# Kernel tuning notes

Measured on AMD Instinct MI355X. Metric: run time of the kernel, lower is better.

## Reference

```python
import jax, jax.numpy as jnp
import numpy as np
from jax import lax

WINDOW_SIZE = 11
SIGMA = 1.5
MAX_VAL = 1.0
C1 = (MAX_VAL * 0.01) ** 2
C2 = (MAX_VAL * 0.03) ** 2


def _make_window(channel: int, k: int = WINDOW_SIZE, sigma: float = SIGMA) -> np.ndarray:
    x = np.arange(k, dtype=np.float64)
    g = np.exp(-((x - k // 2) ** 2) / (2.0 * sigma ** 2))
    g = (g / g.sum()).astype(np.float32)
    # rank-1 separable 3D window, built as dense [C,1,k,k,k] kernel (OIDHW, groups=C)
    w3 = g[:, None, None] * g[None, :, None] * g[None, None, :]
    return np.broadcast_to(w3, (channel, 1, k, k, k)).copy()


def _dwconv3d(x, kernel, pad):
    # depthwise 3D conv, SAME padding for odd kernel
    return lax.conv_general_dilated(
        x, kernel, window_strides=(1, 1, 1), padding=[(pad, pad)] * 3,
        dimension_numbers=("NCDHW", "OIDHW", "NCDHW"),
        feature_group_count=kernel.shape[0])


def setup_inputs() -> dict:
    key = jax.random.key(0)
    k1, k2 = jax.random.split(key)
    shape = (2, 4, 64, 160, 160)  # [B, C, D, H, W]
    img1 = jax.random.uniform(k1, shape, dtype=jnp.float32)
    img2 = jax.random.uniform(k2, shape, dtype=jnp.float32)
    return {"img1": img1, "img2": img2}


def reference(img1, img2):
    channel = img1.shape[1]
    window = jnp.asarray(_make_window(channel))
    pad = WINDOW_SIZE // 2
    # mask = ones_like(img1) in the original -> identity multiply, omitted
    mu1 = _dwconv3d(img1, window, pad)
    mu2 = _dwconv3d(img2, window, pad)
    mu1_sq = mu1 * mu1
    mu2_sq = mu2 * mu2
    mu1_mu2 = mu1 * mu2
    sigma1_sq = _dwconv3d(img1 * img1, window, pad) - mu1_sq
    sigma2_sq = _dwconv3d(img2 * img2, window, pad) - mu2_sq
    sigma12 = _dwconv3d(img1 * img2, window, pad) - mu1_mu2
    ssim_map = ((2.0 * mu1_mu2 + C1) * (2.0 * sigma12 + C2)) / (
        (mu1_sq + mu2_sq + C1) * (sigma1_sq + sigma2_sq + C2))
    ssim = jnp.mean(ssim_map, axis=(0, 2, 3, 4))  # per-channel SSIM, shape [C]
    return 1.0 - ssim
```

## Files before the change

### kernel.cpp

```cpp
#include <hip/hip_runtime.h>
#include <math.h>
#include <stdint.h>
#include <string.h>

typedef float v2f __attribute__((ext_vector_type(2)));

namespace {

constexpr int C_DIM = 4;
constexpr int D_DIM = 64;
constexpr int H_DIM = 160;
constexpr int W_DIM = 160;

constexpr int TH = 16;
constexpr int TW = 16;
constexpr int HALO = 5;
constexpr int EH = 26;
constexpr int EW = 26;
constexpr int QST = 27;
constexpr int MST = 17;
constexpr int NPIX = EH * EW;

constexpr int TILES_W = 10;
constexpr int TPC = 100;
constexpr int NBLOCKS = 2 * C_DIM * TPC;

constexpr float C1f = 1e-4f;
constexpr float C2f = 9e-4f;
constexpr float INV_N = 1.0f / (2.0f * 64.0f * 160.0f * 160.0f);

struct GW { double gd[11]; };

}

static __device__ __forceinline__ void pk_fma(v2f& acc, v2f x, double g) {
    asm("v_pk_fma_f32 %0, %1, %2, %0" : "+v"(acc) : "v"(x), "s"(g));
}

__global__ void finalize_kernel(const float* __restrict__ partial,
                                float* __restrict__ out) {
    const int tid = threadIdx.x;
    const int c = tid >> 6;
    const int lane = tid & 63;
    float s = 0.0f;
#pragma unroll
    for (int b = 0; b < 2; ++b) {
        const int base = (b * C_DIM + c) * TPC;
        s += partial[base + lane];
        if (lane < TPC - 64) s += partial[base + 64 + lane];
    }
#pragma unroll
    for (int off = 32; off > 0; off >>= 1) s += __shfl_down(s, off, 64);
    if (lane == 0 && c < C_DIM) out[c] = 1.0f - s * INV_N;
}

__global__ __launch_bounds__(256, 4) void ssim3d_kernel(
    const float* __restrict__ img1, const float* __restrict__ img2,
    float* __restrict__ partial, GW gwp) {

    const int bid = blockIdx.x;
    const int tile = bid % TPC;
    const int c = (bid / TPC) % C_DIM;
    const int b = bid / (TPC * C_DIM);
    const int h0 = (tile / TILES_W) * TH;
    const int w0 = (tile % TILES_W) * TW;

    const long planeHW = (long)H_DIM * W_DIM;
    const long volbase = (long)(b * C_DIM + c) * D_DIM * planeHW;
    const long org = volbase + (long)(h0 - HALO) * W_DIM + (w0 - HALO);
    const float* __restrict__ p1 = img1 + org;
    const float* __restrict__ p2 = img2 + org;

    const bool interior = (h0 >= HALO) && (h0 + TH + HALO <= H_DIM) &&
                          (w0 >= HALO) && (w0 + TW + HALO <= W_DIM);

    __shared__ float4 xyqp[2][EH][QST];
    __shared__ float4 mid[2][EH][MST];
    __shared__ float  rbuf[4];

    const int tid = threadIdx.x;

    int off_[3], loff_[3];
    unsigned okmask = 0;
#pragma unroll
    for (int k = 0; k < 3; ++k) {
        const int e = tid + k * 256;
        const int hh = e / EW;
        const int ww = e - hh * EW;
        off_[k] = hh * W_DIM + ww;
        loff_[k] = hh * QST + ww;
        const int gh = h0 - HALO + hh;
        const int gw = w0 - HALO + ww;
        if (((unsigned)gh < (unsigned)H_DIM) &&
            ((unsigned)gw < (unsigned)W_DIM))
            okmask |= 1u << k;
    }
    const bool live2 = (tid < NPIX - 512);

    auto fetch_slice = [&](int s, v2f lv[3]) {
        const long sb = (long)s * planeHW;
#pragma unroll
        for (int k = 0; k < 3; ++k) {
            lv[k] = (v2f){0.0f, 0.0f};
            const bool live = (k < 2) || live2;
            if (live && (interior || ((okmask >> k) & 1u))) {
                const long gi = sb + off_[k];
                lv[k].x = p1[gi];
                lv[k].y = p2[gi];
            }
        }
    };
    auto commit_slice = [&](int buf, const v2f lv[3]) {
        float4* base = &xyqp[buf][0][0];
#pragma unroll
        for (int k = 0; k < 3; ++k) {
            const bool live = (k < 2) || live2;
            if (live) {
                const float x = lv[k].x, y = lv[k].y;
                base[loff_[k]] = make_float4(x, y, fmaf(x, x, y * y), x * y);
            }
        }
    };

    const bool wactive = (tid < 208);
    const int whh = tid % 26;
    const int wg2 = (tid / 26) * 2;

    auto wconv = [&](int cur) {
        v2f a0 = {0.f,0.f}, a1 = {0.f,0.f};
        v2f q0 = {0.f,0.f}, q1 = {0.f,0.f};
#pragma unroll
        for (int t = 0; t < 12; ++t) {
            const float4 m = xyqp[cur][whh][wg2 + t];
            const v2f xv = {m.x, m.y};
            const v2f qp = {m.z, m.w};
            if (t <= 10) {
                pk_fma(a0, xv, gwp.gd[t]);
                pk_fma(q0, qp, gwp.gd[t]);
            }
            if (t >= 1) {
                pk_fma(a1, xv, gwp.gd[t-1]);
                pk_fma(q1, qp, gwp.gd[t-1]);
            }
        }
        mid[cur][whh][wg2]     = make_float4(a0.x, a0.y, q0.x, q0.y);
        mid[cur][whh][wg2 + 1] = make_float4(a1.x, a1.y, q1.x, q1.y);
    };

    const int hw = tid & 15;
    const int hy = tid >> 4;

    float accum = 0.0f;
    auto ssim_add = [&](v2f mxy, v2f mqp) {
        const float m1 = mxy.x, m2 = mxy.y;
        const float q = mqp.x, pp = mqp.y;
        const float m1s = m1 * m1;
        const float m2s = m2 * m2;
        const float m12 = m1 * m2;
        const float spp = q - m1s - m2s;
        const float s12 = pp - m12;
        const float num = (2.0f * m12 + C1f) * (2.0f * s12 + C2f);
        const float den = (m1s + m2s + C1f) * (spp + C2f);
        accum = fmaf(num, __builtin_amdgcn_rcpf(den), accum);
    };

    v2f w0xy[14], w0qp[14];
#pragma unroll
    for (int i = 0; i < 14; ++i) {
        w0xy[i] = (v2f){0.f, 0.f}; w0qp[i] = (v2f){0.f, 0.f};
    }

    {
        v2f lv[3];
        fetch_slice(0, lv);
        commit_slice(0, lv);
    }
    __syncthreads();

    for (int sb = 0; sb < D_DIM; sb += 4) {
#pragma unroll
        for (int u = 0; u < 4; ++u) {
            const int s = sb + u;
            v2f lv[3];
            const bool have_next = (s + 1 < D_DIM);
            if (have_next) fetch_slice(s + 1, lv);
            if (wactive) wconv(u & 1);
            if (have_next) commit_slice((u + 1) & 1, lv);
            __syncthreads();
            {
                v2f zx = {0.f,0.f}, zq = {0.f,0.f};
#pragma unroll
                for (int t = 0; t < 11; ++t) {
                    const float4 m = mid[u & 1][hy + t][hw];
                    const v2f ma = {m.x, m.y};
                    const v2f mb = {m.z, m.w};
                    pk_fma(zx, ma, gwp.gd[t]);
                    pk_fma(zq, mb, gwp.gd[t]);
                }
                w0xy[10 + u] = zx; w0qp[10 + u] = zq;
                if (s >= HALO) {
                    v2f mx0 = {0.f,0.f}, mq0 = {0.f,0.f};
#pragma unroll
                    for (int t = 0; t < 11; ++t) {
                        pk_fma(mx0, w0xy[u + t], gwp.gd[t]);
                        pk_fma(mq0, w0qp[u + t], gwp.gd[t]);
                    }
                    ssim_add(mx0, mq0);
                }
            }
        }
        {
#pragma unroll
            for (int k = 0; k < 10; ++k) {
                w0xy[k] = w0xy[k + 4]; w0qp[k] = w0qp[k + 4];
            }
        }
    }

    {
#pragma unroll
        for (int i = 10; i < 14; ++i) {
            w0xy[i] = (v2f){0.f, 0.f}; w0qp[i] = (v2f){0.f, 0.f};
        }
#pragma unroll
        for (int u2 = 0; u2 < 5; ++u2) {
            v2f mx0 = {0.f,0.f}, mq0 = {0.f,0.f};
#pragma unroll
            for (int t = 0; t < 11; ++t) {
                if (u2 + t <= 13) {
                    pk_fma(mx0, w0xy[u2 + t], gwp.gd[t]);
                    pk_fma(mq0, w0qp[u2 + t], gwp.gd[t]);
                }
            }
            ssim_add(mx0, mq0);
        }
    }

#pragma unroll
    for (int off = 32; off > 0; off >>= 1) accum += __shfl_down(accum, off, 64);
    const int wave = tid >> 6;
    const int lane = tid & 63;
    if (lane == 0) rbuf[wave] = accum;
    __syncthreads();
    if (tid == 0) partial[bid] = rbuf[0] + rbuf[1] + rbuf[2] + rbuf[3];
}

extern "C" void kernel_launch(void* const* d_in, const int* in_sizes, int n_in,
                              void* d_out, int out_size, void* d_ws, size_t ws_size,
                              hipStream_t stream) {
    const float* img1 = (const float*)d_in[0];
    const float* img2 = (const float*)d_in[1];
    float* out = (float*)d_out;
    float* partial = (float*)d_ws;

    GW gw;
    {
        double gd[11];
        double ssum = 0.0;
        for (int i = 0; i < 11; ++i) {
            const double t = (double)(i - 5);
            gd[i] = exp(-(t * t) / 4.5);
            ssum += gd[i];
        }
        for (int i = 0; i < 11; ++i) {
            const float gf = (float)(gd[i] / ssum);
            uint32_t ub;
            memcpy(&ub, &gf, 4);
            const uint64_t up = ((uint64_t)ub << 32) | ub;
            memcpy(&gw.gd[i], &up, 8);
        }
    }

    ssim3d_kernel<<<NBLOCKS, 256, 0, stream>>>(img1, img2, partial, gw);
    finalize_kernel<<<1, 256, 0, stream>>>(partial, out);
}
```

Before: 218.7 us.

## Split depth into two chunks per tile and single-buffer the input slice

Each (batch, channel, tile) block is split into two depth halves, so the grid has twice as many blocks. Each half recomputes a halo of slices (aligned down to a multiple of 4) so its sliding-window state is correct at the boundary, and the finalize kernel sums the extra partials. The double-buffered input slice array in shared memory becomes a single buffer, with an extra barrier per slice so the commit runs after the horizontal pass. Launch bounds are raised to 5 blocks per SM. The aim is better CU fill and occupancy, paid for with redundant halo slices and more synchronisation.

Measured after the change: 223.8 us. +2.4%, slower.

```diff
diff --git a/kernel.cpp b/kernel.cpp
--- a/kernel.cpp
+++ b/kernel.cpp
@@ -23,7 +23,9 @@
 
 constexpr int TILES_W = 10;
 constexpr int TPC = 100;
-constexpr int NBLOCKS = 2 * C_DIM * TPC;
+constexpr int D_SPLIT = 2;
+constexpr int DCH = D_DIM / D_SPLIT;
+constexpr int NBLOCKS = D_SPLIT * 2 * C_DIM * TPC;
 
 constexpr float C1f = 1e-4f;
 constexpr float C2f = 9e-4f;
@@ -44,8 +46,8 @@
     const int lane = tid & 63;
     float s = 0.0f;
 #pragma unroll
-    for (int b = 0; b < 2; ++b) {
-        const int base = (b * C_DIM + c) * TPC;
+    for (int r = 0; r < D_SPLIT * 2; ++r) {
+        const int base = (r * C_DIM + c) * TPC;
         s += partial[base + lane];
         if (lane < TPC - 64) s += partial[base + 64 + lane];
     }
@@ -54,16 +56,23 @@
     if (lane == 0 && c < C_DIM) out[c] = 1.0f - s * INV_N;
 }
 
-__global__ __launch_bounds__(256, 4) void ssim3d_kernel(
+__global__ __launch_bounds__(256, 5) void ssim3d_kernel(
     const float* __restrict__ img1, const float* __restrict__ img2,
     float* __restrict__ partial, GW gwp) {
 
     const int bid = blockIdx.x;
     const int tile = bid % TPC;
     const int c = (bid / TPC) % C_DIM;
-    const int b = bid / (TPC * C_DIM);
+    const int rest = bid / (TPC * C_DIM);
+    const int b = rest & 1;
+    const int dh = rest >> 1;
     const int h0 = (tile / TILES_W) * TH;
     const int w0 = (tile % TILES_W) * TW;
+
+    const int d_lo = dh * DCH;
+    const int s_base = (d_lo == 0) ? 0 : ((d_lo - HALO) & ~3);
+    const int s_hi = min(D_DIM - 1, d_lo + DCH - 1 + HALO);
+    const bool has_tail = (d_lo + DCH == D_DIM);
 
     const long planeHW = (long)H_DIM * W_DIM;
     const long volbase = (long)(b * C_DIM + c) * D_DIM * planeHW;
@@ -74,7 +83,7 @@
     const bool interior = (h0 >= HALO) && (h0 + TH + HALO <= H_DIM) &&
                           (w0 >= HALO) && (w0 + TW + HALO <= W_DIM);
 
-    __shared__ float4 xyqp[2][EH][QST];
+    __shared__ float4 xyqp[EH][QST];
     __shared__ float4 mid[2][EH][MST];
     __shared__ float  rbuf[4];
 
@@ -110,8 +119,8 @@
             }
         }
     };
-    auto commit_slice = [&](int buf, const v2f lv[3]) {
-        float4* base = &xyqp[buf][0][0];
+    auto commit_slice = [&](const v2f lv[3]) {
+        float4* base = &xyqp[0][0];
 #pragma unroll
         for (int k = 0; k < 3; ++k) {
             const bool live = (k < 2) || live2;
@@ -131,7 +140,7 @@
         v2f q0 = {0.f,0.f}, q1 = {0.f,0.f};
 #pragma unroll
         for (int t = 0; t < 12; ++t) {
-            const float4 m = xyqp[cur][whh][wg2 + t];
+            const float4 m = xyqp[whh][wg2 + t];
             const v2f xv = {m.x, m.y};
             const v2f qp = {m.z, m.w};
             if (t <= 10) {
@@ -170,23 +179,21 @@
         w0xy[i] = (v2f){0.f, 0.f}; w0qp[i] = (v2f){0.f, 0.f};
     }
 
-    {
-        v2f lv[3];
-        fetch_slice(0, lv);
-        commit_slice(0, lv);
-    }
+    v2f lv[3];
+    fetch_slice(s_base, lv);
+    commit_slice(lv);
     __syncthreads();
 
-    for (int sb = 0; sb < D_DIM; sb += 4) {
+    for (int sb = s_base; sb <= s_hi; sb += 4) {
 #pragma unroll
         for (int u = 0; u < 4; ++u) {
             const int s = sb + u;
-            v2f lv[3];
-            const bool have_next = (s + 1 < D_DIM);
+            if (s > s_hi) break;
+            const bool have_next = (s + 1 <= s_hi);
             if (have_next) fetch_slice(s + 1, lv);
             if (wactive) wconv(u & 1);
-            if (have_next) commit_slice((u + 1) & 1, lv);
             __syncthreads();
+            if (have_next) commit_slice(lv);
             {
                 v2f zx = {0.f,0.f}, zq = {0.f,0.f};
 #pragma unroll
@@ -198,7 +205,7 @@
                     pk_fma(zq, mb, gwp.gd[t]);
                 }
                 w0xy[10 + u] = zx; w0qp[10 + u] = zq;
-                if (s >= HALO) {
+                if (s >= d_lo + HALO) {
                     v2f mx0 = {0.f,0.f}, mq0 = {0.f,0.f};
 #pragma unroll
                     for (int t = 0; t < 11; ++t) {
@@ -208,6 +215,7 @@
                     ssim_add(mx0, mq0);
                 }
             }
+            __syncthreads();
         }
         {
 #pragma unroll
@@ -217,7 +225,7 @@
         }
     }
 
-    {
+    if (has_tail) {
 #pragma unroll
         for (int i = 10; i < 14; ++i) {
             w0xy[i] = (v2f){0.f, 0.f}; w0qp[i] = (v2f){0.f, 0.f};
```

## Store raw xy in single LDS buffer, compute squares in W-pass, 4 outputs per thread

Applied to the files above, without the earlier changes.

The input slice buffer shrinks from double-buffered float4 (x,y,q,p) to a single-buffered v2f of raw values. The squared and product terms are now recomputed inside the W-direction convolution. Each W-pass thread produces four outputs instead of two, so only 104 threads are active there, which gives more register reuse of loaded values. Single buffering requires an extra __syncthreads per slice and moves the commit after the first barrier. It also adds recomputation of q/p and halves W-pass parallelism.

Result: no change. 221.9 us (+1.5%).

```diff
diff --git a/kernel.cpp b/kernel.cpp
--- a/kernel.cpp
+++ b/kernel.cpp
@@ -17,7 +17,7 @@
 constexpr int HALO = 5;
 constexpr int EH = 26;
 constexpr int EW = 26;
-constexpr int QST = 27;
+constexpr int XST = 27;
 constexpr int MST = 17;
 constexpr int NPIX = EH * EW;
 
@@ -44,8 +44,8 @@
     const int lane = tid & 63;
     float s = 0.0f;
 #pragma unroll
-    for (int b = 0; b < 2; ++b) {
-        const int base = (b * C_DIM + c) * TPC;
+    for (int r = 0; r < 2; ++r) {
+        const int base = (r * C_DIM + c) * TPC;
         s += partial[base + lane];
         if (lane < TPC - 64) s += partial[base + 64 + lane];
     }
@@ -74,7 +74,7 @@
     const bool interior = (h0 >= HALO) && (h0 + TH + HALO <= H_DIM) &&
                           (w0 >= HALO) && (w0 + TW + HALO <= W_DIM);
 
-    __shared__ float4 xyqp[2][EH][QST];
+    __shared__ v2f    xy[EH][XST];
     __shared__ float4 mid[2][EH][MST];
     __shared__ float  rbuf[4];
 
@@ -88,7 +88,7 @@
         const int hh = e / EW;
         const int ww = e - hh * EW;
         off_[k] = hh * W_DIM + ww;
-        loff_[k] = hh * QST + ww;
+        loff_[k] = hh * XST + ww;
         const int gh = h0 - HALO + hh;
         const int gw = w0 - HALO + ww;
         if (((unsigned)gh < (unsigned)H_DIM) &&
@@ -110,41 +110,49 @@
             }
         }
     };
-    auto commit_slice = [&](int buf, const v2f lv[3]) {
-        float4* base = &xyqp[buf][0][0];
+    auto commit_slice = [&](const v2f lv[3]) {
+        v2f* base = &xy[0][0];
 #pragma unroll
         for (int k = 0; k < 3; ++k) {
             const bool live = (k < 2) || live2;
-            if (live) {
-                const float x = lv[k].x, y = lv[k].y;
-                base[loff_[k]] = make_float4(x, y, fmaf(x, x, y * y), x * y);
-            }
-        }
-    };
-
-    const bool wactive = (tid < 208);
+            if (live) base[loff_[k]] = lv[k];
+        }
+    };
+
+    const bool wactive = (tid < 104);
     const int whh = tid % 26;
-    const int wg2 = (tid / 26) * 2;
+    const int wg  = (tid / 26) * 4;
 
     auto wconv = [&](int cur) {
-        v2f a0 = {0.f,0.f}, a1 = {0.f,0.f};
-        v2f q0 = {0.f,0.f}, q1 = {0.f,0.f};
-#pragma unroll
-        for (int t = 0; t < 12; ++t) {
-            const float4 m = xyqp[cur][whh][wg2 + t];
-            const v2f xv = {m.x, m.y};
-            const v2f qp = {m.z, m.w};
+        v2f a0 = {0.f,0.f}, a1 = {0.f,0.f}, a2 = {0.f,0.f}, a3 = {0.f,0.f};
+        v2f q0 = {0.f,0.f}, q1 = {0.f,0.f}, q2 = {0.f,0.f}, q3 = {0.f,0.f};
+#pragma unroll
+        for (int t = 0; t < 14; ++t) {
+            const v2f xv = xy[whh][wg + t];
+            v2f qp;
+            qp.x = fmaf(xv.x, xv.x, xv.y * xv.y);
+            qp.y = xv.x * xv.y;
             if (t <= 10) {
                 pk_fma(a0, xv, gwp.gd[t]);
                 pk_fma(q0, qp, gwp.gd[t]);
             }
-            if (t >= 1) {
+            if (t >= 1 && t <= 11) {
                 pk_fma(a1, xv, gwp.gd[t-1]);
                 pk_fma(q1, qp, gwp.gd[t-1]);
             }
-        }
-        mid[cur][whh][wg2]     = make_float4(a0.x, a0.y, q0.x, q0.y);
-        mid[cur][whh][wg2 + 1] = make_float4(a1.x, a1.y, q1.x, q1.y);
+            if (t >= 2 && t <= 12) {
+                pk_fma(a2, xv, gwp.gd[t-2]);
+                pk_fma(q2, qp, gwp.gd[t-2]);
+            }
+            if (t >= 3) {
+                pk_fma(a3, xv, gwp.gd[t-3]);
+                pk_fma(q3, qp, gwp.gd[t-3]);
+            }
+        }
+        mid[cur][whh][wg]     = make_float4(a0.x, a0.y, q0.x, q0.y);
+        mid[cur][whh][wg + 1] = make_float4(a1.x, a1.y, q1.x, q1.y);
+        mid[cur][whh][wg + 2] = make_float4(a2.x, a2.y, q2.x, q2.y);
+        mid[cur][whh][wg + 3] = make_float4(a3.x, a3.y, q3.x, q3.y);
     };
 
     const int hw = tid & 15;
@@ -170,23 +178,20 @@
         w0xy[i] = (v2f){0.f, 0.f}; w0qp[i] = (v2f){0.f, 0.f};
     }
 
-    {
-        v2f lv[3];
-        fetch_slice(0, lv);
-        commit_slice(0, lv);
-    }
+    v2f lv[3];
+    fetch_slice(0, lv);
+    commit_slice(lv);
     __syncthreads();
 
     for (int sb = 0; sb < D_DIM; sb += 4) {
 #pragma unroll
         for (int u = 0; u < 4; ++u) {
             const int s = sb + u;
-            v2f lv[3];
             const bool have_next = (s + 1 < D_DIM);
             if (have_next) fetch_slice(s + 1, lv);
             if (wactive) wconv(u & 1);
-            if (have_next) commit_slice((u + 1) & 1, lv);
             __syncthreads();
+            if (have_next) commit_slice(lv);
             {
                 v2f zx = {0.f,0.f}, zq = {0.f,0.f};
 #pragma unroll
@@ -208,6 +213,7 @@
                     ssim_add(mx0, mq0);
                 }
             }
+            __syncthreads();
         }
         {
 #pragma unroll
```
